# Performance work log

Hardware: AMD Instinct MI355X
Metric: run time of the kernel (lower is better)

The kernel has to match this reference:

```python
import jax, jax.numpy as jnp
import numpy as np

B, IMG, P, D, H, HD, DEPTH, MLPD = 32, 224, 16, 768, 12, 64, 12, 3072
N = (IMG // P) ** 2 + 1  # 197 tokens incl. cls
TASKS, PL, NPL = 10, 5, 5
SCALE = HD ** -0.5


def _ln(x, w, b, eps=1e-6):
    m = jnp.mean(x, -1, keepdims=True)
    v = jnp.var(x, -1, keepdims=True)
    return (x - m) * jax.lax.rsqrt(v + eps) * w + b


def setup_inputs():
    key = jax.random.key(0)
    ks = jax.random.split(key, 16)
    g = lambda k, shape: (jax.random.normal(k, shape) * 0.02).astype(jnp.float32)
    return dict(
        x=jax.random.normal(ks[0], (B, 3, IMG, IMG), jnp.float32),
        task_id=jax.random.randint(ks[1], (B,), 0, TASKS),
        patch_w=g(ks[2], (D, 3, P, P)), patch_b=jnp.zeros((D,), jnp.float32),
        cls_token=g(ks[3], (1, 1, D)), pos_embed=g(ks[4], (1, N, D)),
        ln1_w=jnp.ones((DEPTH, D)), ln1_b=jnp.zeros((DEPTH, D)),
        qkv_w=g(ks[5], (DEPTH, 3 * D, D)), qkv_b=jnp.zeros((DEPTH, 3 * D)),
        proj_w=g(ks[6], (DEPTH, D, D)), proj_b=jnp.zeros((DEPTH, D)),
        ln2_w=jnp.ones((DEPTH, D)), ln2_b=jnp.zeros((DEPTH, D)),
        fc1_w=g(ks[7], (DEPTH, MLPD, D)), fc1_b=jnp.zeros((DEPTH, MLPD)),
        fc2_w=g(ks[8], (DEPTH, D, MLPD)), fc2_b=jnp.zeros((DEPTH, D)),
        norm_w=jnp.ones((D,)), norm_b=jnp.zeros((D,)),
        prefix_k=g(ks[9], (NPL, TASKS, PL, H, HD)),
        prefix_v=g(ks[10], (NPL, TASKS, PL, H, HD)),
        act_scale=jnp.ones((NPL, 2, 1, 1), jnp.float32),
    )


def reference(x, task_id, patch_w, patch_b, cls_token, pos_embed, ln1_w, ln1_b,
              qkv_w, qkv_b, proj_w, proj_b, ln2_w, ln2_b, fc1_w, fc1_b,
              fc2_w, fc2_b, norm_w, norm_b, prefix_k, prefix_v, act_scale):
    tid = jnp.clip(task_id, 0, TASKS - 1)
    Bx = x.shape[0]
    # patch embed: conv stride P -> [B, D, 14, 14] -> [B, 196, D]
    h = jax.lax.conv_general_dilated(x, patch_w, (P, P), 'VALID',
                                     dimension_numbers=('NCHW', 'OIHW', 'NCHW'))
    h = h.reshape(Bx, D, -1).transpose(0, 2, 1) + patch_b
    h = jnp.concatenate([jnp.broadcast_to(cls_token, (Bx, 1, D)), h], axis=1)
    h = h + pos_embed
    for i in range(DEPTH):
        xn = _ln(h, ln1_w[i], ln1_b[i])
        qkv = (xn @ qkv_w[i].T + qkv_b[i]).reshape(Bx, N, 3, H, HD)
        q, k, v = [jnp.transpose(qkv[:, :, j], (0, 2, 1, 3)) for j in range(3)]  # [B,H,N,HD]
        if i < NPL:
            kp = jnp.transpose(prefix_k[i][tid], (0, 2, 1, 3))  # [B,H,PL,HD]
            vp = jnp.transpose(prefix_v[i][tid], (0, 2, 1, 3))
            k = jnp.concatenate([kp, k], axis=2)
            v = jnp.concatenate([vp, v], axis=2)
        logits = jnp.einsum('bhqd,bhkd->bhqk', q, k) * SCALE
        if i < NPL:
            s = act_scale[i]  # [2,1,1]
            pp = logits[..., :PL]
            pp = pp + jax.nn.sigmoid(pp * s[0]) * s[1]  # norga gating on prefix logits
            logits = jnp.concatenate([pp, logits[..., PL:]], axis=-1)
        probs = jax.nn.softmax(logits, axis=-1)
        attn = jnp.einsum('bhqk,bhkd->bhqd', probs, v)
        attn = attn.transpose(0, 2, 1, 3).reshape(Bx, N, D)
        h = h + attn @ proj_w[i].T + proj_b[i]
        yn = _ln(h, ln2_w[i], ln2_b[i])
        y = jax.nn.gelu(yn @ fc1_w[i].T + fc1_b[i], approximate=False)
        h = h + y @ fc2_w[i].T + fc2_b[i]
    h = _ln(h, norm_w, norm_b)
    return h[:, 0]
```

## Files before the change

### kernel.cpp

```cpp
#include <hip/hip_runtime.h>
#include <hip/hip_bf16.h>

#define B_     32
#define NTOK   197
#define NPATCH 196
#define D_     768
#define H_     12
#define HD_    64
#define DEPTH_ 12
#define MLPD_  3072
#define TASKS_ 10
#define PL_    5
#define NPL_   5
#define SCALE_ 0.125f
#define ROWS   (B_*NTOK)
#define PSZ    (ROWS*D_)

typedef unsigned short ushortT;
typedef __bf16 bf16x8 __attribute__((ext_vector_type(8)));
typedef float  f32x4  __attribute__((ext_vector_type(4)));
typedef unsigned int u32x4 __attribute__((ext_vector_type(4)));

union FragU { u32x4 u; bf16x8 b; };

__device__ inline unsigned int f2bf(float f){
  unsigned int u = __float_as_uint(f);
  return (u + 0x7fffu + ((u >> 16) & 1u)) >> 16;
}
__device__ inline float bflo(unsigned int u){ return __uint_as_float(u << 16); }
__device__ inline float bfhi(unsigned int u){ return __uint_as_float(u & 0xffff0000u); }
__device__ inline float gelu_f(float x){ return 0.5f * x * (1.f + erff(x * 0.70710678118f)); }

__device__ inline void gload16(const void* g, void* l){
  __builtin_amdgcn_global_load_lds(
      (const __attribute__((address_space(1))) void*)(uintptr_t)g,
      (__attribute__((address_space(3))) void*)(uintptr_t)l,
      16, 0, 0);
}

#define DSREAD(dst, addr, OFFS) \
  asm volatile("ds_read_b128 %0, %1 offset:" OFFS : "=v"(dst) : "v"(addr))

__global__ __launch_bounds__(256) void convw4_kernel(const float* __restrict__ s0,
    const float* __restrict__ s1, const float* __restrict__ s2, const float* __restrict__ s3,
    ushortT* __restrict__ dst)
{
  int idx = blockIdx.x * 256 + threadIdx.x;
  int e = idx * 8;
  if (e >= 7077888) return;
  const float* s; int loc;
  if (e < 1769472)      { s = s0; loc = e; }
  else if (e < 2359296) { s = s1; loc = e - 1769472; }
  else if (e < 4718592) { s = s2; loc = e - 2359296; }
  else                  { s = s3; loc = e - 4718592; }
  float4 a = *(const float4*)(s + loc);
  float4 c = *(const float4*)(s + loc + 4);
  uint4 o;
  o.x = f2bf(a.x) | (f2bf(a.y) << 16);
  o.y = f2bf(a.z) | (f2bf(a.w) << 16);
  o.z = f2bf(c.x) | (f2bf(c.y) << 16);
  o.w = f2bf(c.z) | (f2bf(c.w) << 16);
  *(uint4*)(dst + e) = o;
}

__global__ __launch_bounds__(256) void convw1_kernel(const float* __restrict__ s,
    ushortT* __restrict__ dst, int n8)
{
  int idx = blockIdx.x * 256 + threadIdx.x;
  if (idx >= n8) return;
  int e = idx * 8;
  float4 a = *(const float4*)(s + e);
  float4 c = *(const float4*)(s + e + 4);
  uint4 o;
  o.x = f2bf(a.x) | (f2bf(a.y) << 16);
  o.y = f2bf(a.z) | (f2bf(a.w) << 16);
  o.z = f2bf(c.x) | (f2bf(c.y) << 16);
  o.w = f2bf(c.z) | (f2bf(c.w) << 16);
  *(uint4*)(dst + e) = o;
}

__global__ __launch_bounds__(256) void im2col_kernel(const float* __restrict__ x,
                                                     ushortT* __restrict__ out)
{
  int idx = blockIdx.x * 256 + threadIdx.x;
  const int tot = B_ * NPATCH * D_;
  if (idx >= tot) return;
  int m = idx / D_, k = idx - m * D_;
  int b = m / NPATCH, p = m - b * NPATCH;
  int pr = p / 14, pc = p - pr * 14;
  int c = k >> 8, r = k & 255;
  int py = r >> 4, px = r & 15;
  float v = x[(((size_t)(b * 3 + c) * 224) + pr * 16 + py) * 224 + pc * 16 + px];
  out[idx] = (ushortT)f2bf(v);
}

__global__ __launch_bounds__(256) void assemble_kernel(const float* __restrict__ pe,
    const float* __restrict__ patch_b, const float* __restrict__ cls,
    const float* __restrict__ pos, float* __restrict__ h)
{
  int idx = blockIdx.x * 256 + threadIdx.x;
  const int tot = ROWS * D_;
  if (idx >= tot) return;
  int bn = idx / D_, d = idx - bn * D_;
  int b = bn / NTOK, n = bn - b * NTOK;
  float v;
  if (n == 0) v = cls[d];
  else        v = pe[((size_t)b * NPATCH + (n - 1)) * D_ + d] + patch_b[d];
  h[idx] = v + pos[(size_t)n * D_ + d];
}

__global__ __launch_bounds__(256) void reduce3_kernel(
    const ushortT* __restrict__ p, const float* __restrict__ bias,
    float* __restrict__ h)
{
  int idx = blockIdx.x * 256 + threadIdx.x;
  int e = idx * 8;
  int n = e % D_;
  uint4 a = *(const uint4*)(p + e);
  uint4 b = *(const uint4*)(p + PSZ + e);
  uint4 c = *(const uint4*)(p + 2 * PSZ + e);
  float4 h0 = *(const float4*)(h + e);
  float4 h1 = *(const float4*)(h + e + 4);
  float4 bb0 = *(const float4*)(bias + n);
  float4 bb1 = *(const float4*)(bias + n + 4);
  float r0 = h0.x + bb0.x + bflo(a.x) + bflo(b.x) + bflo(c.x);
  float r1 = h0.y + bb0.y + bfhi(a.x) + bfhi(b.x) + bfhi(c.x);
  float r2 = h0.z + bb0.z + bflo(a.y) + bflo(b.y) + bflo(c.y);
  float r3 = h0.w + bb0.w + bfhi(a.y) + bfhi(b.y) + bfhi(c.y);
  float r4 = h1.x + bb1.x + bflo(a.z) + bflo(b.z) + bflo(c.z);
  float r5 = h1.y + bb1.y + bfhi(a.z) + bfhi(b.z) + bfhi(c.z);
  float r6 = h1.z + bb1.z + bflo(a.w) + bflo(b.w) + bflo(c.w);
  float r7 = h1.w + bb1.w + bfhi(a.w) + bfhi(b.w) + bfhi(c.w);
  *(float4*)(h + e)     = (float4){r0, r1, r2, r3};
  *(float4*)(h + e + 4) = (float4){r4, r5, r6, r7};
}

template<int OUTBF>
__global__ __launch_bounds__(256) void ln_kernel(const float* __restrict__ x, size_t xstride,
    const float* __restrict__ w, const float* __restrict__ b,
    void* __restrict__ y, size_t ystride)
{
  const float* xr = x + (size_t)blockIdx.x * xstride;
  float vals[3];
  float s = 0.f, ss = 0.f;
  #pragma unroll
  for (int t = 0; t < 3; t++) {
    float v = xr[threadIdx.x + t * 256];
    vals[t] = v; s += v; ss += v * v;
  }
  #pragma unroll
  for (int off = 32; off >= 1; off >>= 1) {
    s  += __shfl_down(s, off);
    ss += __shfl_down(ss, off);
  }
  __shared__ float sm[4], ssm[4];
  int wid = threadIdx.x >> 6, lane = threadIdx.x & 63;
  if (lane == 0) { sm[wid] = s; ssm[wid] = ss; }
  __syncthreads();
  s  = sm[0] + sm[1] + sm[2] + sm[3];
  ss = ssm[0] + ssm[1] + ssm[2] + ssm[3];
  float mean = s * (1.f / D_);
  float var  = ss * (1.f / D_) - mean * mean;
  float inv  = rsqrtf(var + 1e-6f);
  #pragma unroll
  for (int t = 0; t < 3; t++) {
    int d = threadIdx.x + t * 256;
    float v = (vals[t] - mean) * inv * w[d] + b[d];
    if (OUTBF) ((ushortT*)y)[(size_t)blockIdx.x * ystride + d] = (ushortT)f2bf(v);
    else       ((float*)y)  [(size_t)blockIdx.x * ystride + d] = v;
  }
}

template<int OUTBF, int ACT, int HASRES>
__global__ __launch_bounds__(256, 5) void gemm_mfma(
    const ushortT* __restrict__ A, const ushortT* __restrict__ W,
    const float* __restrict__ bias, const float* __restrict__ resid,
    void* __restrict__ Cout, int M, int N, int K, int LDA, int LDW)
{
  __shared__ ushortT lds[12288];
  const int tid = threadIdx.x, lane = tid & 63, wid = tid >> 6;
  const int bm = blockIdx.y * 128, bn = blockIdx.x * 64;
  const int wm = (wid >> 1) * 64, wn = (wid & 1) * 32;
  const int kz = blockIdx.z;
  A += (size_t)kz * K; W += (size_t)kz * K;
  char* Cb = (char*)Cout + (size_t)kz * M * N * (OUTBF ? 2 : 4);

  const int srow = lane >> 2;
  const int scol = ((lane & 3) ^ ((lane >> 3) & 3)) * 8;
  int arow0 = bm + (2 * wid) * 16 + srow;     if (arow0 > M - 1) arow0 = M - 1;
  int arow1 = bm + (2 * wid + 1) * 16 + srow; if (arow1 > M - 1) arow1 = M - 1;
  const int wrow = bn + wid * 16 + srow;
  const ushortT* aP0 = A + (size_t)arow0 * LDA + scol;
  const ushortT* aP1 = A + (size_t)arow1 * LDA + scol;
  const ushortT* wP0 = W + (size_t)wrow * LDW + scol;
  ushortT* sA = lds + 2 * wid * 512;
  ushortT* sW = lds + 8192 + wid * 512;

  f32x4 acc[4][2];
  #pragma unroll
  for (int i = 0; i < 4; i++)
    #pragma unroll
    for (int j = 0; j < 2; j++)
      acc[i][j] = (f32x4){0.f, 0.f, 0.f, 0.f};

  const int rsel = lane & 15, kc = lane >> 4;
  const unsigned ldsbase = (unsigned)(size_t)&lds[0];
  const unsigned rowoff = (unsigned)(rsel * 64 + ((kc ^ ((rsel >> 1) & 3)) << 4));
  const unsigned aBase = ldsbase + (unsigned)(wm * 64) + rowoff;
  const unsigned bBase = ldsbase + 16384u + (unsigned)(wn * 64) + rowoff;

  const int nk = K >> 5;

  #pragma unroll
  for (int p = 0; p < 2; ++p) {
    const int off = p * 32;
    gload16(aP0 + off, sA + p * 4096); gload16(aP1 + off, sA + p * 4096 + 512);
    gload16(wP0 + off, sW + p * 2048);
  }

  for (int kt = 0; kt < nk; ++kt) {
    const int cb = kt & 1;
    asm volatile("s_waitcnt vmcnt(3)" ::: "memory");
    __builtin_amdgcn_sched_barrier(0);
    __builtin_amdgcn_s_barrier();

    const unsigned aAddr = aBase + (unsigned)cb * 8192u;
    const unsigned bAddr = bBase + (unsigned)cb * 4096u;
    FragU fa0, fa1, fa2, fa3, fb0, fb1;
    DSREAD(fa0.u, aAddr, "0");
    DSREAD(fa1.u, aAddr, "1024");
    DSREAD(fa2.u, aAddr, "2048");
    DSREAD(fa3.u, aAddr, "3072");
    DSREAD(fb0.u, bAddr, "0");
    DSREAD(fb1.u, bAddr, "1024");
    asm volatile("s_waitcnt lgkmcnt(0)" ::: "memory");
    __builtin_amdgcn_sched_barrier(0);
    __builtin_amdgcn_s_barrier();

    const int nt = kt + 2;
    const int off = (nt < nk) ? nt * 32 : 0;
    gload16(aP0 + off, sA + cb * 4096); gload16(aP1 + off, sA + cb * 4096 + 512);
    gload16(wP0 + off, sW + cb * 2048);

    acc[0][0] = __builtin_amdgcn_mfma_f32_16x16x32_bf16(fa0.b, fb0.b, acc[0][0], 0, 0, 0);
    acc[0][1] = __builtin_amdgcn_mfma_f32_16x16x32_bf16(fa0.b, fb1.b, acc[0][1], 0, 0, 0);
    acc[1][0] = __builtin_amdgcn_mfma_f32_16x16x32_bf16(fa1.b, fb0.b, acc[1][0], 0, 0, 0);
    acc[1][1] = __builtin_amdgcn_mfma_f32_16x16x32_bf16(fa1.b, fb1.b, acc[1][1], 0, 0, 0);
    acc[2][0] = __builtin_amdgcn_mfma_f32_16x16x32_bf16(fa2.b, fb0.b, acc[2][0], 0, 0, 0);
    acc[2][1] = __builtin_amdgcn_mfma_f32_16x16x32_bf16(fa2.b, fb1.b, acc[2][1], 0, 0, 0);
    acc[3][0] = __builtin_amdgcn_mfma_f32_16x16x32_bf16(fa3.b, fb0.b, acc[3][0], 0, 0, 0);
    acc[3][1] = __builtin_amdgcn_mfma_f32_16x16x32_bf16(fa3.b, fb1.b, acc[3][1], 0, 0, 0);
  }

  const int crow = (lane >> 4) * 4, ccol = lane & 15;
  #pragma unroll
  for (int i = 0; i < 4; i++) {
    #pragma unroll
    for (int r = 0; r < 4; r++) {
      int m = bm + wm + i * 16 + crow + r;
      if (m < M) {
        #pragma unroll
        for (int j = 0; j < 2; j++) {
          int n = bn + wn + j * 16 + ccol;
          float v = acc[i][j][r];
          if (bias) v += bias[n];
          if (ACT) v = gelu_f(v);
          if (HASRES) v += resid[(size_t)m * N + n];
          if (OUTBF) ((ushortT*)Cb)[(size_t)m * N + n] = (ushortT)f2bf(v);
          else       ((float*)Cb)  [(size_t)m * N + n] = v;
        }
      }
    }
  }
  asm volatile("s_waitcnt vmcnt(0)" ::: "memory");
}

#define KROWS 208
#define VSTR  232
__global__ __launch_bounds__(256) void attn_mfma(
    const ushortT* __restrict__ qkv, const float* __restrict__ prefix_k,
    const float* __restrict__ prefix_v, const float* __restrict__ act_scale,
    const int* __restrict__ task_id, ushortT* __restrict__ out,
    int layer, int koff)
{
  __shared__ ushortT smem[13312 + 14848 + 4096];
  ushortT* Kl = smem;
  ushortT* Vt = smem + 13312;
  ushortT* Ps = smem + 13312 + 14848;

  const int tid = threadIdx.x, lane = tid & 63, wid = tid >> 6;
  const int g = lane >> 4, qc = lane & 15;
  const int qh = blockIdx.x, h = blockIdx.y, b = blockIdx.z;
  const int KtA = NTOK + koff;

  int tsk = 0;
  float s0 = 1.f, s1 = 1.f;
  if (koff) {
    tsk = task_id[b]; tsk = tsk < 0 ? 0 : (tsk > TASKS_ - 1 ? TASKS_ - 1 : tsk);
    s0 = act_scale[layer * 2]; s1 = act_scale[layer * 2 + 1];
  }

  {
    uint4* vz = (uint4*)Vt;
    for (int i = tid; i < 14848 / 8; i += 256) vz[i] = (uint4){0, 0, 0, 0};
    uint4* kz = (uint4*)(Kl + 202 * 64);
    if (tid < 48) kz[tid] = (uint4){0, 0, 0, 0};
  }
  __syncthreads();

  for (int u = tid; u < KtA * 8; u += 256) {
    int row = u >> 3, cg = u & 7;
    uint4 val;
    if (row < koff) {
      size_t off = ((((size_t)layer * TASKS_ + tsk) * PL_ + row) * H_ + h) * HD_ + cg * 8;
      float4 f0 = *(const float4*)(prefix_k + off);
      float4 f1 = *(const float4*)(prefix_k + off + 4);
      val.x = f2bf(f0.x) | (f2bf(f0.y) << 16); val.y = f2bf(f0.z) | (f2bf(f0.w) << 16);
      val.z = f2bf(f1.x) | (f2bf(f1.y) << 16); val.w = f2bf(f1.z) | (f2bf(f1.w) << 16);
    } else {
      int n = row - koff;
      val = *(const uint4*)(qkv + ((size_t)b * NTOK + n) * 2304 + D_ + h * HD_ + cg * 8);
    }
    *(uint4*)(Kl + row * 64 + ((cg * 8) ^ ((row & 7) << 3))) = val;
  }
  for (int u = tid; u < KtA * 8; u += 256) {
    int row = u >> 3, dg = u & 7;
    ushortT e[8];
    if (row < koff) {
      size_t off = ((((size_t)layer * TASKS_ + tsk) * PL_ + row) * H_ + h) * HD_ + dg * 8;
      #pragma unroll
      for (int t = 0; t < 8; t++) e[t] = (ushortT)f2bf(prefix_v[off + t]);
    } else {
      int n = row - koff;
      uint4 v = *(const uint4*)(qkv + ((size_t)b * NTOK + n) * 2304 + 2 * D_ + h * HD_ + dg * 8);
      *(uint4*)e = v;
    }
    #pragma unroll
    for (int t = 0; t < 8; t++) Vt[(dg * 8 + t) * VSTR + row] = e[t];
  }
  __syncthreads();

  const int tend = qh ? 13 : 7;
  for (int t = qh * 7 + wid; t < tend; t += 4) {
    const int q0 = t * 16;
    int qr = q0 + qc; if (qr > NTOK - 1) qr = NTOK - 1;
    const ushortT* qp = qkv + ((size_t)b * NTOK + qr) * 2304 + h * HD_ + g * 8;
    bf16x8 qf0 = *(const bf16x8*)qp;
    bf16x8 qf1 = *(const bf16x8*)(qp + 32);

    f32x4 sacc[13];
    #pragma unroll
    for (int kt = 0; kt < 13; kt++) sacc[kt] = (f32x4){0.f, 0.f, 0.f, 0.f};
    #pragma unroll
    for (int kt = 0; kt < 13; kt++) {
      int row = kt * 16 + qc;
      int sw = (row & 7) << 3;
      bf16x8 ka0 = *(const bf16x8*)(Kl + row * 64 + ((g * 8) ^ sw));
      bf16x8 ka1 = *(const bf16x8*)(Kl + row * 64 + ((32 + g * 8) ^ sw));
      sacc[kt] = __builtin_amdgcn_mfma_f32_16x16x32_bf16(ka0, qf0, sacc[kt], 0, 0, 0);
      sacc[kt] = __builtin_amdgcn_mfma_f32_16x16x32_bf16(ka1, qf1, sacc[kt], 0, 0, 0);
    }

    float* sp = (float*)sacc;
    float mx = -1e30f;
    #pragma unroll
    for (int kt = 0; kt < 13; kt++)
      #pragma unroll
      for (int r = 0; r < 4; r++) {
        int k = kt * 16 + g * 4 + r;
        float s = sp[kt * 4 + r] * SCALE_;
        if (koff && k < PL_) s += s1 / (1.f + __expf(-s * s0));
        if (k >= KtA) s = -1e30f;
        sp[kt * 4 + r] = s;
        mx = fmaxf(mx, s);
      }
    mx = fmaxf(mx, __shfl_xor(mx, 16));
    mx = fmaxf(mx, __shfl_xor(mx, 32));
    float sum = 0.f;
    #pragma unroll
    for (int i = 0; i < 52; i++) { float p = __expf(sp[i] - mx); sp[i] = p; sum += p; }
    sum += __shfl_xor(sum, 16);
    sum += __shfl_xor(sum, 32);
    const float inv = 1.f / sum;

    f32x4 oacc[4];
    #pragma unroll
    for (int d = 0; d < 4; d++) oacc[d] = (f32x4){0.f, 0.f, 0.f, 0.f};
    #pragma unroll
    for (int c = 0; c < 7; c++) {
      ushortT* slab = Ps + wid * 1024 + (c & 1) * 512;
      uint2 w0, w1;
      {
        float p0 = sp[8 * c + 0] * inv, p1 = sp[8 * c + 1] * inv;
        float p2 = sp[8 * c + 2] * inv, p3 = sp[8 * c + 3] * inv;
        w0.x = f2bf(p0) | (f2bf(p1) << 16); w0.y = f2bf(p2) | (f2bf(p3) << 16);
      }
      if (c < 6) {
        float p0 = sp[8 * c + 4] * inv, p1 = sp[8 * c + 5] * inv;
        float p2 = sp[8 * c + 6] * inv, p3 = sp[8 * c + 7] * inv;
        w1.x = f2bf(p0) | (f2bf(p1) << 16); w1.y = f2bf(p2) | (f2bf(p3) << 16);
      } else { w1.x = 0; w1.y = 0; }
      *(uint2*)(slab + qc * 32 + g * 4) = w0;
      *(uint2*)(slab + qc * 32 + 16 + g * 4) = w1;
      bf16x8 pa = *(const bf16x8*)(slab + qc * 32 + g * 8);
      #pragma unroll
      for (int dt = 0; dt < 4; dt++) {
        bf16x8 vb = *(const bf16x8*)(Vt + (dt * 16 + qc) * VSTR + c * 32 + g * 8);
        oacc[dt] = __builtin_amdgcn_mfma_f32_16x16x32_bf16(pa, vb, oacc[dt], 0, 0, 0);
      }
    }

    #pragma unroll
    for (int r = 0; r < 4; r++) {
      int q = q0 + g * 4 + r;
      if (q < NTOK) {
        size_t ro = ((size_t)b * NTOK + q) * D_ + h * HD_;
        #pragma unroll
        for (int dt = 0; dt < 4; dt++)
          out[ro + dt * 16 + qc] = (ushortT)f2bf(oacc[dt][r]);
      }
    }
  }
}

extern "C" void kernel_launch(void* const* d_in, const int* in_sizes, int n_in,
                              void* d_out, int out_size, void* d_ws, size_t ws_size,
                              hipStream_t stream)
{
  (void)in_sizes; (void)n_in; (void)out_size; (void)ws_size;
  const float* x         = (const float*)d_in[0];
  const int*   task_id   = (const int*)  d_in[1];
  const float* patch_w   = (const float*)d_in[2];
  const float* patch_b   = (const float*)d_in[3];
  const float* cls_token = (const float*)d_in[4];
  const float* pos_embed = (const float*)d_in[5];
  const float* ln1_w     = (const float*)d_in[6];
  const float* ln1_b     = (const float*)d_in[7];
  const float* qkv_w     = (const float*)d_in[8];
  const float* qkv_b     = (const float*)d_in[9];
  const float* proj_w    = (const float*)d_in[10];
  const float* proj_b    = (const float*)d_in[11];
  const float* ln2_w     = (const float*)d_in[12];
  const float* ln2_b     = (const float*)d_in[13];
  const float* fc1_w     = (const float*)d_in[14];
  const float* fc1_b     = (const float*)d_in[15];
  const float* fc2_w     = (const float*)d_in[16];
  const float* fc2_b     = (const float*)d_in[17];
  const float* norm_w    = (const float*)d_in[18];
  const float* norm_b    = (const float*)d_in[19];
  const float* prefix_k  = (const float*)d_in[20];
  const float* prefix_v  = (const float*)d_in[21];
  const float* act_scale = (const float*)d_in[22];
  float* out = (float*)d_out;

  char* wsb = (char*)d_ws;
  float*   h      = (float*)  (wsb);
  ushortT* actA   = (ushortT*)(wsb + 19365888);
  ushortT* qkvbuf = (ushortT*)(wsb + 29048832);
  ushortT* mlpbuf = (ushortT*)(wsb + 58097664);
  ushortT* wsc    = (ushortT*)(wsb + 96829440);
  float*   peout  = (float*)qkvbuf;

  ushortT* wqkv  = wsc;
  ushortT* wproj = wsc + 1769472;
  ushortT* wfc1  = wsc + 2359296;
  ushortT* wfc2  = wsc + 4718592;

  convw1_kernel<<<288, 256, 0, stream>>>(patch_w, wsc, 73728);
  im2col_kernel<<<(B_ * NPATCH * D_ + 255) / 256, 256, 0, stream>>>(x, actA);
  gemm_mfma<0,0,0><<<dim3(12, 49), 256, 0, stream>>>(
      actA, wsc, nullptr, nullptr, peout, B_ * NPATCH, D_, D_, D_, D_);
  assemble_kernel<<<(ROWS * D_ + 255) / 256, 256, 0, stream>>>(
      peout, patch_b, cls_token, pos_embed, h);

  for (int i = 0; i < DEPTH_; i++) {
    convw4_kernel<<<3456, 256, 0, stream>>>(
        qkv_w + (size_t)i * 1769472, proj_w + (size_t)i * 589824,
        fc1_w + (size_t)i * 2359296, fc2_w + (size_t)i * 2359296, wsc);
    ln_kernel<1><<<ROWS, 256, 0, stream>>>(h, D_, ln1_w + i * D_, ln1_b + i * D_, actA, D_);
    gemm_mfma<1,0,0><<<dim3(36, 50), 256, 0, stream>>>(
        actA, wqkv, qkv_b + i * 3 * D_, nullptr, qkvbuf, ROWS, 3 * D_, D_, D_, D_);
    attn_mfma<<<dim3(2, H_, B_), 256, 0, stream>>>(
        qkvbuf, prefix_k, prefix_v, act_scale, task_id, actA, i, (i < NPL_) ? PL_ : 0);
    gemm_mfma<0,0,1><<<dim3(12, 50), 256, 0, stream>>>(
        actA, wproj, proj_b + i * D_, h, h, ROWS, D_, D_, D_, D_);
    ln_kernel<1><<<ROWS, 256, 0, stream>>>(h, D_, ln2_w + i * D_, ln2_b + i * D_, actA, D_);
    gemm_mfma<1,1,0><<<dim3(48, 50), 256, 0, stream>>>(
        actA, wfc1, fc1_b + i * MLPD_, nullptr, mlpbuf, ROWS, MLPD_, D_, D_, D_);
    gemm_mfma<1,0,0><<<dim3(12, 50, 3), 256, 0, stream>>>(
        mlpbuf, wfc2, nullptr, nullptr, qkvbuf, ROWS, D_, MLPD_ / 3, MLPD_, MLPD_);
    reduce3_kernel<<<PSZ / 8 / 256, 256, 0, stream>>>(qkvbuf, fc2_b + i * D_, h);
  }

  ln_kernel<0><<<B_, 256, 0, stream>>>(h, (size_t)NTOK * D_, norm_w, norm_b, out, D_);
}
```

Baseline: 3.342 ms.

## Add 256x256-tile 512-thread GEMM kernel for QKV, FC1 and FC2

Adds a new gemm_wide kernel that uses 256x256 output tiles with 8 waves, each wave computing 128x64, plus triple-buffered LDS staging with swizzled layout and split MFMA phases interleaved with global loads. The QKV, FC1 and split-K FC2 GEMMs now use it in place of the 128x128 kernel. Larger tiles raise arithmetic intensity and cut redundant global and LDS traffic. The cost is fewer blocks (225, 300 and 225), which may underfill 256 CUs and leave tail waste on M=6304, and higher register pressure.

After: 4.013 ms. +20.1%, slower.

```diff
diff --git a/kernel.cpp b/kernel.cpp
--- a/kernel.cpp
+++ b/kernel.cpp
@@ -266,6 +266,151 @@
           if (bias) v += bias[n];
           if (ACT) v = gelu_f(v);
           if (HASRES) v += resid[(size_t)m * N + n];
+          if (OUTBF) ((ushortT*)Cb)[(size_t)m * N + n] = (ushortT)f2bf(v);
+          else       ((float*)Cb)  [(size_t)m * N + n] = v;
+        }
+      }
+    }
+  }
+  asm volatile("s_waitcnt vmcnt(0)" ::: "memory");
+}
+
+template<int OUTBF, int ACT>
+__global__ __launch_bounds__(512, 2) void gemm_wide(
+    const ushortT* __restrict__ A, const ushortT* __restrict__ W,
+    const float* __restrict__ bias,
+    void* __restrict__ Cout, int M, int N, int K, int LDA, int LDW)
+{
+  __shared__ ushortT lds[49152];
+  const int tid = threadIdx.x, lane = tid & 63, wid = tid >> 6;
+  const int bm = blockIdx.y * 256, bn = blockIdx.x * 256;
+  const int wm = (wid >> 2) * 128, wn = (wid & 3) * 64;
+  const int kz = blockIdx.z;
+  A += (size_t)kz * K; W += (size_t)kz * K;
+  char* Cb = (char*)Cout + (size_t)kz * M * N * (OUTBF ? 2 : 4);
+
+  const int srow = lane >> 2;
+  const int scol = ((lane & 3) ^ ((lane >> 3) & 3)) * 8;
+  int arow0 = bm + (2 * wid) * 16 + srow;     if (arow0 > M - 1) arow0 = M - 1;
+  int arow1 = bm + (2 * wid + 1) * 16 + srow; if (arow1 > M - 1) arow1 = M - 1;
+  const int wrow0 = bn + (2 * wid) * 16 + srow;
+  const int wrow1 = bn + (2 * wid + 1) * 16 + srow;
+  const ushortT* aP0 = A + (size_t)arow0 * LDA + scol;
+  const ushortT* aP1 = A + (size_t)arow1 * LDA + scol;
+  const ushortT* wP0 = W + (size_t)wrow0 * LDW + scol;
+  const ushortT* wP1 = W + (size_t)wrow1 * LDW + scol;
+  ushortT* sA = lds + 2 * wid * 512;
+  ushortT* sW = lds + 24576 + 2 * wid * 512;
+
+  f32x4 acc[8][4];
+  #pragma unroll
+  for (int i = 0; i < 8; i++)
+    #pragma unroll
+    for (int j = 0; j < 4; j++)
+      acc[i][j] = (f32x4){0.f, 0.f, 0.f, 0.f};
+
+  const int rsel = lane & 15, kc = lane >> 4;
+  const unsigned ldsbase = (unsigned)(size_t)&lds[0];
+  const unsigned rowoff = (unsigned)(rsel * 64 + ((kc ^ ((rsel >> 1) & 3)) << 4));
+  const unsigned aBase = ldsbase + (unsigned)(wm * 64) + rowoff;
+  const unsigned bBase = ldsbase + 49152u + (unsigned)(wn * 64) + rowoff;
+
+  const int nk = K >> 5;
+
+  #pragma unroll
+  for (int p = 0; p < 2; ++p) {
+    const int off = p * 32;
+    gload16(aP0 + off, sA + p * 8192); gload16(aP1 + off, sA + p * 8192 + 512);
+    gload16(wP0 + off, sW + p * 8192); gload16(wP1 + off, sW + p * 8192 + 512);
+  }
+
+  int cb = 0;
+  int rb = 2;
+  for (int kt = 0; kt < nk; ++kt) {
+    asm volatile("s_waitcnt vmcnt(4)" ::: "memory");
+    __builtin_amdgcn_sched_barrier(0);
+    __builtin_amdgcn_s_barrier();
+
+    const int nt = kt + 2;
+    const int off = (nt < nk) ? nt * 32 : 0;
+    const unsigned aAddr = aBase + (unsigned)cb * 16384u;
+    const unsigned bAddr = bBase + (unsigned)cb * 16384u;
+
+    gload16(aP0 + off, sA + rb * 8192); gload16(aP1 + off, sA + rb * 8192 + 512);
+    FragU b0, b1, b2, b3, a0, a1, a2, a3;
+    DSREAD(b0.u, bAddr, "0");
+    DSREAD(b1.u, bAddr, "1024");
+    DSREAD(b2.u, bAddr, "2048");
+    DSREAD(b3.u, bAddr, "3072");
+    DSREAD(a0.u, aAddr, "0");
+    DSREAD(a1.u, aAddr, "1024");
+    DSREAD(a2.u, aAddr, "2048");
+    DSREAD(a3.u, aAddr, "3072");
+    asm volatile("s_waitcnt lgkmcnt(0)" ::: "memory");
+    __builtin_amdgcn_sched_barrier(0);
+    __builtin_amdgcn_s_setprio(1);
+    acc[0][0] = __builtin_amdgcn_mfma_f32_16x16x32_bf16(a0.b, b0.b, acc[0][0], 0, 0, 0);
+    acc[0][1] = __builtin_amdgcn_mfma_f32_16x16x32_bf16(a0.b, b1.b, acc[0][1], 0, 0, 0);
+    acc[0][2] = __builtin_amdgcn_mfma_f32_16x16x32_bf16(a0.b, b2.b, acc[0][2], 0, 0, 0);
+    acc[0][3] = __builtin_amdgcn_mfma_f32_16x16x32_bf16(a0.b, b3.b, acc[0][3], 0, 0, 0);
+    acc[1][0] = __builtin_amdgcn_mfma_f32_16x16x32_bf16(a1.b, b0.b, acc[1][0], 0, 0, 0);
+    acc[1][1] = __builtin_amdgcn_mfma_f32_16x16x32_bf16(a1.b, b1.b, acc[1][1], 0, 0, 0);
+    acc[1][2] = __builtin_amdgcn_mfma_f32_16x16x32_bf16(a1.b, b2.b, acc[1][2], 0, 0, 0);
+    acc[1][3] = __builtin_amdgcn_mfma_f32_16x16x32_bf16(a1.b, b3.b, acc[1][3], 0, 0, 0);
+    acc[2][0] = __builtin_amdgcn_mfma_f32_16x16x32_bf16(a2.b, b0.b, acc[2][0], 0, 0, 0);
+    acc[2][1] = __builtin_amdgcn_mfma_f32_16x16x32_bf16(a2.b, b1.b, acc[2][1], 0, 0, 0);
+    acc[2][2] = __builtin_amdgcn_mfma_f32_16x16x32_bf16(a2.b, b2.b, acc[2][2], 0, 0, 0);
+    acc[2][3] = __builtin_amdgcn_mfma_f32_16x16x32_bf16(a2.b, b3.b, acc[2][3], 0, 0, 0);
+    acc[3][0] = __builtin_amdgcn_mfma_f32_16x16x32_bf16(a3.b, b0.b, acc[3][0], 0, 0, 0);
+    acc[3][1] = __builtin_amdgcn_mfma_f32_16x16x32_bf16(a3.b, b1.b, acc[3][1], 0, 0, 0);
+    acc[3][2] = __builtin_amdgcn_mfma_f32_16x16x32_bf16(a3.b, b2.b, acc[3][2], 0, 0, 0);
+    acc[3][3] = __builtin_amdgcn_mfma_f32_16x16x32_bf16(a3.b, b3.b, acc[3][3], 0, 0, 0);
+    __builtin_amdgcn_s_setprio(0);
+
+    gload16(wP0 + off, sW + rb * 8192); gload16(wP1 + off, sW + rb * 8192 + 512);
+    FragU a4, a5, a6, a7;
+    DSREAD(a4.u, aAddr, "4096");
+    DSREAD(a5.u, aAddr, "5120");
+    DSREAD(a6.u, aAddr, "6144");
+    DSREAD(a7.u, aAddr, "7168");
+    asm volatile("s_waitcnt lgkmcnt(0)" ::: "memory");
+    __builtin_amdgcn_sched_barrier(0);
+    __builtin_amdgcn_s_setprio(1);
+    acc[4][0] = __builtin_amdgcn_mfma_f32_16x16x32_bf16(a4.b, b0.b, acc[4][0], 0, 0, 0);
+    acc[4][1] = __builtin_amdgcn_mfma_f32_16x16x32_bf16(a4.b, b1.b, acc[4][1], 0, 0, 0);
+    acc[4][2] = __builtin_amdgcn_mfma_f32_16x16x32_bf16(a4.b, b2.b, acc[4][2], 0, 0, 0);
+    acc[4][3] = __builtin_amdgcn_mfma_f32_16x16x32_bf16(a4.b, b3.b, acc[4][3], 0, 0, 0);
+    acc[5][0] = __builtin_amdgcn_mfma_f32_16x16x32_bf16(a5.b, b0.b, acc[5][0], 0, 0, 0);
+    acc[5][1] = __builtin_amdgcn_mfma_f32_16x16x32_bf16(a5.b, b1.b, acc[5][1], 0, 0, 0);
+    acc[5][2] = __builtin_amdgcn_mfma_f32_16x16x32_bf16(a5.b, b2.b, acc[5][2], 0, 0, 0);
+    acc[5][3] = __builtin_amdgcn_mfma_f32_16x16x32_bf16(a5.b, b3.b, acc[5][3], 0, 0, 0);
+    acc[6][0] = __builtin_amdgcn_mfma_f32_16x16x32_bf16(a6.b, b0.b, acc[6][0], 0, 0, 0);
+    acc[6][1] = __builtin_amdgcn_mfma_f32_16x16x32_bf16(a6.b, b1.b, acc[6][1], 0, 0, 0);
+    acc[6][2] = __builtin_amdgcn_mfma_f32_16x16x32_bf16(a6.b, b2.b, acc[6][2], 0, 0, 0);
+    acc[6][3] = __builtin_amdgcn_mfma_f32_16x16x32_bf16(a6.b, b3.b, acc[6][3], 0, 0, 0);
+    acc[7][0] = __builtin_amdgcn_mfma_f32_16x16x32_bf16(a7.b, b0.b, acc[7][0], 0, 0, 0);
+    acc[7][1] = __builtin_amdgcn_mfma_f32_16x16x32_bf16(a7.b, b1.b, acc[7][1], 0, 0, 0);
+    acc[7][2] = __builtin_amdgcn_mfma_f32_16x16x32_bf16(a7.b, b2.b, acc[7][2], 0, 0, 0);
+    acc[7][3] = __builtin_amdgcn_mfma_f32_16x16x32_bf16(a7.b, b3.b, acc[7][3], 0, 0, 0);
+    __builtin_amdgcn_s_setprio(0);
+
+    cb = (cb == 2) ? 0 : cb + 1;
+    rb = (rb == 2) ? 0 : rb + 1;
+  }
+
+  const int crow = (lane >> 4) * 4, ccol = lane & 15;
+  #pragma unroll
+  for (int i = 0; i < 8; i++) {
+    #pragma unroll
+    for (int r = 0; r < 4; r++) {
+      int m = bm + wm + i * 16 + crow + r;
+      if (m < M) {
+        #pragma unroll
+        for (int j = 0; j < 4; j++) {
+          int n = bn + wn + j * 16 + ccol;
+          float v = acc[i][j][r];
+          if (bias) v += bias[n];
+          if (ACT) v = gelu_f(v);
           if (OUTBF) ((ushortT*)Cb)[(size_t)m * N + n] = (ushortT)f2bf(v);
           else       ((float*)Cb)  [(size_t)m * N + n] = v;
         }
@@ -478,17 +623,17 @@
         qkv_w + (size_t)i * 1769472, proj_w + (size_t)i * 589824,
         fc1_w + (size_t)i * 2359296, fc2_w + (size_t)i * 2359296, wsc);
     ln_kernel<1><<<ROWS, 256, 0, stream>>>(h, D_, ln1_w + i * D_, ln1_b + i * D_, actA, D_);
-    gemm_mfma<1,0,0><<<dim3(36, 50), 256, 0, stream>>>(
-        actA, wqkv, qkv_b + i * 3 * D_, nullptr, qkvbuf, ROWS, 3 * D_, D_, D_, D_);
+    gemm_wide<1,0><<<dim3(9, 25), 512, 0, stream>>>(
+        actA, wqkv, qkv_b + i * 3 * D_, qkvbuf, ROWS, 3 * D_, D_, D_, D_);
     attn_mfma<<<dim3(2, H_, B_), 256, 0, stream>>>(
         qkvbuf, prefix_k, prefix_v, act_scale, task_id, actA, i, (i < NPL_) ? PL_ : 0);
     gemm_mfma<0,0,1><<<dim3(12, 50), 256, 0, stream>>>(
         actA, wproj, proj_b + i * D_, h, h, ROWS, D_, D_, D_, D_);
     ln_kernel<1><<<ROWS, 256, 0, stream>>>(h, D_, ln2_w + i * D_, ln2_b + i * D_, actA, D_);
-    gemm_mfma<1,1,0><<<dim3(48, 50), 256, 0, stream>>>(
-        actA, wfc1, fc1_b + i * MLPD_, nullptr, mlpbuf, ROWS, MLPD_, D_, D_, D_);
-    gemm_mfma<1,0,0><<<dim3(12, 50, 3), 256, 0, stream>>>(
-        mlpbuf, wfc2, nullptr, nullptr, qkvbuf, ROWS, D_, MLPD_ / 3, MLPD_, MLPD_);
+    gemm_wide<1,1><<<dim3(12, 25), 512, 0, stream>>>(
+        actA, wfc1, fc1_b + i * MLPD_, mlpbuf, ROWS, MLPD_, D_, D_, D_);
+    gemm_wide<1,0><<<dim3(3, 25, 3), 512, 0, stream>>>(
+        mlpbuf, wfc2, nullptr, qkvbuf, ROWS, D_, MLPD_ / 3, MLPD_, MLPD_);
     reduce3_kernel<<<PSZ / 8 / 256, 256, 0, stream>>>(qkvbuf, fc2_b + i * D_, h);
   }
 
```

## Fuse split-K reductions with following LayerNorm and split proj GEMM over K

Applied to the files above, without the earlier changes.

Replaces the separate residual-reduce and LayerNorm kernels with one per-row kernel that sums the split-K bf16 partials, adds bias and residual, writes h, and emits the next LayerNorm's bf16 output. The proj GEMM becomes a 2-way split-K into bf16 partials instead of a fused residual epilogue, which adds parallelism but adds a partial round-trip and bf16 rounding of the partials. The first ln1 is hoisted before the loop, and the GEMM launch bound is raised to 6 waves per SIMD, which may add register pressure.

After: 3.179 ms. -4.9%, faster.

```diff
diff --git a/kernel.cpp b/kernel.cpp
--- a/kernel.cpp
+++ b/kernel.cpp
@@ -27,8 +27,7 @@
   unsigned int u = __float_as_uint(f);
   return (u + 0x7fffu + ((u >> 16) & 1u)) >> 16;
 }
-__device__ inline float bflo(unsigned int u){ return __uint_as_float(u << 16); }
-__device__ inline float bfhi(unsigned int u){ return __uint_as_float(u & 0xffff0000u); }
+__device__ inline float bf2f(ushortT u){ return __uint_as_float(((unsigned)u) << 16); }
 __device__ inline float gelu_f(float x){ return 0.5f * x * (1.f + erff(x * 0.70710678118f)); }
 
 __device__ inline void gload16(const void* g, void* l){
@@ -109,30 +108,47 @@
   h[idx] = v + pos[(size_t)n * D_ + d];
 }
 
-__global__ __launch_bounds__(256) void reduce3_kernel(
+template<int NP, int DOLN>
+__global__ __launch_bounds__(256) void reduce_ln_kernel(
     const ushortT* __restrict__ p, const float* __restrict__ bias,
-    float* __restrict__ h)
-{
-  int idx = blockIdx.x * 256 + threadIdx.x;
-  int e = idx * 8;
-  int n = e % D_;
-  uint4 a = *(const uint4*)(p + e);
-  uint4 b = *(const uint4*)(p + PSZ + e);
-  uint4 c = *(const uint4*)(p + 2 * PSZ + e);
-  float4 h0 = *(const float4*)(h + e);
-  float4 h1 = *(const float4*)(h + e + 4);
-  float4 bb0 = *(const float4*)(bias + n);
-  float4 bb1 = *(const float4*)(bias + n + 4);
-  float r0 = h0.x + bb0.x + bflo(a.x) + bflo(b.x) + bflo(c.x);
-  float r1 = h0.y + bb0.y + bfhi(a.x) + bfhi(b.x) + bfhi(c.x);
-  float r2 = h0.z + bb0.z + bflo(a.y) + bflo(b.y) + bflo(c.y);
-  float r3 = h0.w + bb0.w + bfhi(a.y) + bfhi(b.y) + bfhi(c.y);
-  float r4 = h1.x + bb1.x + bflo(a.z) + bflo(b.z) + bflo(c.z);
-  float r5 = h1.y + bb1.y + bfhi(a.z) + bfhi(b.z) + bfhi(c.z);
-  float r6 = h1.z + bb1.z + bflo(a.w) + bflo(b.w) + bflo(c.w);
-  float r7 = h1.w + bb1.w + bfhi(a.w) + bfhi(b.w) + bfhi(c.w);
-  *(float4*)(h + e)     = (float4){r0, r1, r2, r3};
-  *(float4*)(h + e + 4) = (float4){r4, r5, r6, r7};
+    float* __restrict__ h, const float* __restrict__ lw,
+    const float* __restrict__ lb, ushortT* __restrict__ y)
+{
+  const size_t base = (size_t)blockIdx.x * D_;
+  const int t = threadIdx.x;
+  float vals[3];
+  float s = 0.f, ss = 0.f;
+  #pragma unroll
+  for (int e = 0; e < 3; e++) {
+    int d = t + e * 256;
+    size_t idx = base + d;
+    float acc = h[idx] + bias[d];
+    #pragma unroll
+    for (int q = 0; q < NP; q++) acc += bf2f(p[(size_t)q * PSZ + idx]);
+    h[idx] = acc;
+    vals[e] = acc; s += acc; ss += acc * acc;
+  }
+  if (DOLN) {
+    #pragma unroll
+    for (int off = 32; off >= 1; off >>= 1) {
+      s  += __shfl_down(s, off);
+      ss += __shfl_down(ss, off);
+    }
+    __shared__ float sm[4], ssm[4];
+    int wid = t >> 6, lane = t & 63;
+    if (lane == 0) { sm[wid] = s; ssm[wid] = ss; }
+    __syncthreads();
+    s  = sm[0] + sm[1] + sm[2] + sm[3];
+    ss = ssm[0] + ssm[1] + ssm[2] + ssm[3];
+    float mean = s * (1.f / D_);
+    float var  = ss * (1.f / D_) - mean * mean;
+    float inv  = rsqrtf(var + 1e-6f);
+    #pragma unroll
+    for (int e = 0; e < 3; e++) {
+      int d = t + e * 256;
+      y[base + d] = (ushortT)f2bf((vals[e] - mean) * inv * lw[d] + lb[d]);
+    }
+  }
 }
 
 template<int OUTBF>
@@ -172,7 +188,7 @@
 }
 
 template<int OUTBF, int ACT, int HASRES>
-__global__ __launch_bounds__(256, 5) void gemm_mfma(
+__global__ __launch_bounds__(256, 6) void gemm_mfma(
     const ushortT* __restrict__ A, const ushortT* __restrict__ W,
     const float* __restrict__ bias, const float* __restrict__ resid,
     void* __restrict__ Cout, int M, int N, int K, int LDA, int LDW)
@@ -473,23 +489,31 @@
   assemble_kernel<<<(ROWS * D_ + 255) / 256, 256, 0, stream>>>(
       peout, patch_b, cls_token, pos_embed, h);
 
+  ln_kernel<1><<<ROWS, 256, 0, stream>>>(h, D_, ln1_w, ln1_b, actA, D_);
+
   for (int i = 0; i < DEPTH_; i++) {
     convw4_kernel<<<3456, 256, 0, stream>>>(
         qkv_w + (size_t)i * 1769472, proj_w + (size_t)i * 589824,
         fc1_w + (size_t)i * 2359296, fc2_w + (size_t)i * 2359296, wsc);
-    ln_kernel<1><<<ROWS, 256, 0, stream>>>(h, D_, ln1_w + i * D_, ln1_b + i * D_, actA, D_);
     gemm_mfma<1,0,0><<<dim3(36, 50), 256, 0, stream>>>(
         actA, wqkv, qkv_b + i * 3 * D_, nullptr, qkvbuf, ROWS, 3 * D_, D_, D_, D_);
     attn_mfma<<<dim3(2, H_, B_), 256, 0, stream>>>(
         qkvbuf, prefix_k, prefix_v, act_scale, task_id, actA, i, (i < NPL_) ? PL_ : 0);
-    gemm_mfma<0,0,1><<<dim3(12, 50), 256, 0, stream>>>(
-        actA, wproj, proj_b + i * D_, h, h, ROWS, D_, D_, D_, D_);
-    ln_kernel<1><<<ROWS, 256, 0, stream>>>(h, D_, ln2_w + i * D_, ln2_b + i * D_, actA, D_);
+    gemm_mfma<1,0,0><<<dim3(12, 50, 2), 256, 0, stream>>>(
+        actA, wproj, nullptr, nullptr, qkvbuf, ROWS, D_, D_ / 2, D_, D_);
+    reduce_ln_kernel<2,1><<<ROWS, 256, 0, stream>>>(
+        qkvbuf, proj_b + i * D_, h, ln2_w + i * D_, ln2_b + i * D_, actA);
     gemm_mfma<1,1,0><<<dim3(48, 50), 256, 0, stream>>>(
         actA, wfc1, fc1_b + i * MLPD_, nullptr, mlpbuf, ROWS, MLPD_, D_, D_, D_);
     gemm_mfma<1,0,0><<<dim3(12, 50, 3), 256, 0, stream>>>(
         mlpbuf, wfc2, nullptr, nullptr, qkvbuf, ROWS, D_, MLPD_ / 3, MLPD_, MLPD_);
-    reduce3_kernel<<<PSZ / 8 / 256, 256, 0, stream>>>(qkvbuf, fc2_b + i * D_, h);
+    if (i < DEPTH_ - 1) {
+      reduce_ln_kernel<3,1><<<ROWS, 256, 0, stream>>>(
+          qkvbuf, fc2_b + i * D_, h, ln1_w + (i + 1) * D_, ln1_b + (i + 1) * D_, actA);
+    } else {
+      reduce_ln_kernel<3,0><<<ROWS, 256, 0, stream>>>(
+          qkvbuf, fc2_b + i * D_, h, nullptr, nullptr, nullptr);
+    }
   }
 
   ln_kernel<0><<<B_, 256, 0, stream>>>(h, (size_t)NTOK * D_, norm_w, norm_b, out, D_);
```
